# Kernel optimization log

Hardware: AMD Instinct MI355X
Metric: run time of the kernel (lower is better)

## Reference

```python
import jax, jax.numpy as jnp
import numpy as np

N = 200000      # query points
D_IN = 3        # coordinate dims
H = 256         # hidden features
L = 4           # hidden layers (between first and last Perceptron)
S = 8           # n_series == out_features


def setup_inputs() -> dict:
    key = jax.random.key(0)
    ks = jax.random.split(key, 7)
    coords = jax.random.normal(ks[0], (N, D_IN), dtype=jnp.float32)
    # Stacked per-series weights (all series share shapes; original loads the
    # same checkpoint into each, but we use independent random params).
    scale0 = 1.0 / np.sqrt(D_IN)
    scaleh = 1.0 / np.sqrt(H)
    W0 = jax.random.uniform(ks[1], (S, D_IN, H), jnp.float32, -scale0, scale0)
    b0 = jax.random.uniform(ks[2], (S, H), jnp.float32, -scale0, scale0)
    Wh = jax.random.uniform(ks[3], (S, L, H, H), jnp.float32, -scaleh, scaleh)
    bh = jax.random.uniform(ks[4], (S, L, H), jnp.float32, -scaleh, scaleh)
    Wout = jax.random.uniform(ks[5], (S, H, 1), jnp.float32, -scaleh, scaleh)
    bout = jax.random.uniform(ks[6], (S, 1), jnp.float32, -scaleh, scaleh)
    return {"coords": coords, "W0": W0, "b0": b0, "Wh": Wh, "bh": bh,
            "Wout": Wout, "bout": bout}


def reference(coords, W0, b0, Wh, bh, Wout, bout):
    # All S series' MLPs batched into grouped GEMMs (einsum over series axis s).
    # Perceptron = Linear + softplus; last layer is plain Linear.
    h = jax.nn.softplus(jnp.einsum('nd,sdh->snh', coords, W0) + b0[:, None, :])
    for i in range(L):  # small fixed layer count
        h = jax.nn.softplus(
            jnp.einsum('snh,shk->snk', h, Wh[:, i]) + bh[:, i][:, None, :])
    out = jnp.einsum('snh,sho->sno', h, Wout) + bout[:, None, :]  # [S,N,1]
    output = jnp.transpose(out[..., 0], (1, 0))  # concat along dim=1 -> [N,S]
    return (output, coords)
```

## Files before the change

### kernel.cpp

```cpp
#include <hip/hip_runtime.h>
#include <hip/hip_bf16.h>
#include <cstdint>

typedef __attribute__((ext_vector_type(8))) short short8;
typedef __attribute__((ext_vector_type(4))) float float4v;

#define LOG2E 1.44269504088896340736f
#define LN2   0.69314718055994530942f

#if __has_builtin(__builtin_amdgcn_exp2f)
__device__ __forceinline__ float fexp2(float x){ return __builtin_amdgcn_exp2f(x); }
#else
__device__ __forceinline__ float fexp2(float x){ return exp2f(x); }
#endif
#if __has_builtin(__builtin_amdgcn_logf)
__device__ __forceinline__ float flog2(float x){ return __builtin_amdgcn_logf(x); }
#else
__device__ __forceinline__ float flog2(float x){ return log2f(x); }
#endif

__device__ __forceinline__ float softplus_hat(float zh){
  return flog2(1.0f + fexp2(zh));
}

__device__ __forceinline__ unsigned short bf16_trunc(float f){
  return (unsigned short)(__builtin_bit_cast(unsigned int, f) >> 16);
}

#define HSTRIDE 264
#define MISTEP  4288
#define HSIZE   (64 * 264 + 16 * 16)

__global__ void convert_wh(const float* __restrict__ Wh,
                           unsigned short* __restrict__ Wt){
  int e = blockIdx.x * 256 + threadIdx.x;
  int n  = e & 255;
  int k  = (e >> 8) & 255;
  int sl = e >> 16;
  float v = Wh[e];
  __hip_bfloat16 h = __float2bfloat16(v);
  Wt[(sl << 16) + ((k >> 5) << 13) + (n << 5) + (k & 31)] =
      __builtin_bit_cast(unsigned short, h);
}

__device__ __forceinline__ float4v bf16_mfma(short8 a, short8 b, float4v c){
  return __builtin_amdgcn_mfma_f32_16x16x32_bf16(a, b, c, 0, 0, 0);
}

__device__ __forceinline__ void l0_rows(
    unsigned short* __restrict__ ht, const float4v* __restrict__ c4,
    int j, int c, float w0, float w1, float w2, float bb)
{
  float4v x0 = c4[j*3+0], x1 = c4[j*3+1], x2 = c4[j*3+2];
  float z0 = fmaf(x0.z, w2, fmaf(x0.y, w1, fmaf(x0.x, w0, bb)));
  float z1 = fmaf(x1.y, w2, fmaf(x1.x, w1, fmaf(x0.w, w0, bb)));
  float z2 = fmaf(x2.x, w2, fmaf(x1.w, w1, fmaf(x1.z, w0, bb)));
  float z3 = fmaf(x2.w, w2, fmaf(x2.z, w1, fmaf(x2.y, w0, bb)));
  ht[(4*j+0)*HSTRIDE + j*16 + c] = bf16_trunc(softplus_hat(z0));
  ht[(4*j+1)*HSTRIDE + j*16 + c] = bf16_trunc(softplus_hat(z1));
  ht[(4*j+2)*HSTRIDE + j*16 + c] = bf16_trunc(softplus_hat(z2));
  ht[(4*j+3)*HSTRIDE + j*16 + c] = bf16_trunc(softplus_hat(z3));
}

__device__ __forceinline__ void sp2(const float4v (&acc)[4][4],
    unsigned short* __restrict__ cptr, int kb)
{
  #pragma unroll
  for (int t = 0; t < 2; ++t) {
    const int idx = kb * 2 + t, mi = idx >> 2, ni = idx & 3;
    float4v v = acc[mi][ni];
    #pragma unroll
    for (int r = 0; r < 4; ++r)
      cptr[mi * MISTEP + r * HSTRIDE + ni * 16] = bf16_trunc(softplus_hat(v[r]));
  }
}

__device__ __forceinline__ void spdot2(const float4v (&acc)[4][4],
    const float (&wv)[4], float (&p)[16], int kb)
{
  #pragma unroll
  for (int t = 0; t < 2; ++t) {
    const int idx = kb * 2 + t, mi = idx >> 2, ni = idx & 3;
    float4v v = acc[mi][ni];
    #pragma unroll
    for (int r = 0; r < 4; ++r)
      p[mi * 4 + r] = fmaf(softplus_hat(v[r]), wv[ni], p[mi * 4 + r]);
  }
}

template<int PH, bool LOADN, class F>
__device__ __forceinline__ void mfma_phase(
    const unsigned short* __restrict__ bb,
    const unsigned short* __restrict__ bn,
    const unsigned short* __restrict__ aptr,
    short8 (&bq)[3][4], float4v (&acc)[4][4], F&& other)
{
  short8 a0[4], a1[4];
  #pragma unroll
  for (int mi = 0; mi < 4; ++mi)
    a0[mi] = *(const short8*)(aptr + mi * MISTEP);

  #pragma unroll
  for (int kb = 0; kb < 8; ++kb) {
    short8* cur = (kb & 1) ? a1 : a0;
    short8* nxt = (kb & 1) ? a0 : a1;
    if (kb < 7) {
      #pragma unroll
      for (int mi = 0; mi < 4; ++mi)
        nxt[mi] = *(const short8*)(aptr + (kb + 1) * 32 + mi * MISTEP);
    }
    const int slot = (8 * PH + kb) % 3;
    #pragma unroll
    for (int mi = 0; mi < 4; ++mi)
      #pragma unroll
      for (int ni = 0; ni < 4; ++ni)
        acc[mi][ni] = bf16_mfma(cur[mi], bq[slot][ni], acc[mi][ni]);
    if (kb < 5) {
      #pragma unroll
      for (int ni = 0; ni < 4; ++ni)
        bq[slot][ni] = *(const short8*)(bb + (kb + 3) * 8192 + ni * 512);
    } else if (LOADN) {
      #pragma unroll
      for (int ni = 0; ni < 4; ++ni)
        bq[slot][ni] = *(const short8*)(bn + (kb - 5) * 8192 + ni * 512);
    }
    other(kb);
  }
}

__global__ __launch_bounds__(256, 2) void series_mlp(
    const float* __restrict__ coords,
    const float* __restrict__ W0, const float* __restrict__ b0,
    const float* __restrict__ bh,
    const float* __restrict__ Wout, const float* __restrict__ bout,
    const unsigned short* __restrict__ Wt,
    float* __restrict__ out)
{
  __shared__ __align__(16) unsigned short h_lds[2 * HSIZE];
  __shared__ float cbuf[384];

  const int tid  = threadIdx.x;
  const int lane = tid & 63;
  const int wave = tid >> 6;
  const int s    = blockIdx.x & 7;
  const int m0   = (blockIdx.x >> 3) * 128;

  const int q    = lane >> 4;
  const int lr   = lane & 15;
  const int colb = (wave << 6) + lr;

  {
    int i1 = m0 * 3 + tid;
    int i2 = i1 + 256;
    cbuf[tid] = coords[i1 < 599999 ? i1 : 599999];
    if (tid < 128) cbuf[tid + 256] = coords[i2 < 599999 ? i2 : 599999];
  }

  const int c = tid;
  const float w0  = W0[(s * 3 + 0) * 256 + c] * LOG2E;
  const float w1  = W0[(s * 3 + 1) * 256 + c] * LOG2E;
  const float w2  = W0[(s * 3 + 2) * 256 + c] * LOG2E;
  const float bb0 = b0[s * 256 + c] * LOG2E;

  const unsigned short* bbase0 = Wt + ((s << 2) << 16) + (colb << 5) + (q << 3);
  short8 bq[3][4];
  #pragma unroll
  for (int i = 0; i < 3; ++i)
    #pragma unroll
    for (int ni = 0; ni < 4; ++ni)
      bq[i][ni] = *(const short8*)(bbase0 + i * 8192 + ni * 512);

  const unsigned short* aptrA = h_lds + lr * HSTRIDE + (lr >> 2) * 16 + (q << 3);
  const unsigned short* aptrB = aptrA + HSIZE;
  unsigned short* cptrA = h_lds + q * 1072 + colb;
  unsigned short* cptrB = cptrA + HSIZE;

  const float* bh_s = bh + (s << 10);
  const float4v* c4 = (const float4v*)cbuf;

  __syncthreads();
  #pragma unroll
  for (int j = 0; j < 16; ++j)
    l0_rows(h_lds, c4, j, c, w0, w1, w2, bb0);
  __syncthreads();

  float4v accA[4][4], accB[4][4];

#define INIT_ACC(ACC, LIDX)                                                   \
  {                                                                           \
    float bias[4];                                                            \
    _Pragma("unroll")                                                         \
    for (int ni = 0; ni < 4; ++ni)                                            \
      bias[ni] = bh_s[(LIDX) * 256 + colb + ni * 16] * LOG2E;                 \
    _Pragma("unroll")                                                         \
    for (int mi = 0; mi < 4; ++mi)                                            \
      _Pragma("unroll")                                                       \
      for (int ni = 0; ni < 4; ++ni)                                          \
        ACC[mi][ni] = (float4v){bias[ni], bias[ni], bias[ni], bias[ni]};      \
  }

  const unsigned short* B0 = bbase0;
  const unsigned short* B1 = bbase0 + 65536;
  const unsigned short* B2 = bbase0 + 2 * 65536;
  const unsigned short* B3 = bbase0 + 3 * 65536;

  INIT_ACC(accA, 0)
  mfma_phase<0, true>(B0, B0, aptrA, bq, accA, [&](int kb){
    l0_rows(h_lds + HSIZE, c4 + 48, 2 * kb + 0, c, w0, w1, w2, bb0);
    l0_rows(h_lds + HSIZE, c4 + 48, 2 * kb + 1, c, w0, w1, w2, bb0);
  });
  __syncthreads();

  INIT_ACC(accB, 0)
  mfma_phase<1, true>(B0, B1, aptrB, bq, accB,
      [&](int kb){ sp2(accA, cptrA, kb); });
  __syncthreads();

  INIT_ACC(accA, 1)
  mfma_phase<2, true>(B1, B1, aptrA, bq, accA,
      [&](int kb){ sp2(accB, cptrB, kb); });
  __syncthreads();

  INIT_ACC(accB, 1)
  mfma_phase<3, true>(B1, B2, aptrB, bq, accB,
      [&](int kb){ sp2(accA, cptrA, kb); });
  __syncthreads();

  INIT_ACC(accA, 2)
  mfma_phase<4, true>(B2, B2, aptrA, bq, accA,
      [&](int kb){ sp2(accB, cptrB, kb); });
  __syncthreads();

  INIT_ACC(accB, 2)
  mfma_phase<5, true>(B2, B3, aptrB, bq, accB,
      [&](int kb){ sp2(accA, cptrA, kb); });
  __syncthreads();

  INIT_ACC(accA, 3)
  mfma_phase<6, true>(B3, B3, aptrA, bq, accA,
      [&](int kb){ sp2(accB, cptrB, kb); });
  __syncthreads();

  INIT_ACC(accB, 3)
  float wv[4];
  #pragma unroll
  for (int ni = 0; ni < 4; ++ni)
    wv[ni] = Wout[(s << 8) + colb + ni * 16];
  float pA[16], pB[16];
  #pragma unroll
  for (int i = 0; i < 16; ++i) pA[i] = 0.f;
  mfma_phase<7, false>(B3, B3, aptrB, bq, accB,
      [&](int kb){ spdot2(accA, wv, pA, kb); });

  #pragma unroll
  for (int i = 0; i < 16; ++i) pB[i] = 0.f;
  #pragma unroll
  for (int kb = 0; kb < 8; ++kb)
    spdot2(accB, wv, pB, kb);

  __syncthreads();
  float* redA = (float*)h_lds;
  float* redB = redA + 64 * 68;
  #pragma unroll
  for (int mi = 0; mi < 4; ++mi)
    #pragma unroll
    for (int r = 0; r < 4; ++r) {
      int row = mi * 16 + (q << 2) + r;
      redA[row * 68 + (wave << 4) + lr] = pA[mi * 4 + r];
      redB[row * 68 + (wave << 4) + lr] = pB[mi * 4 + r];
    }
  __syncthreads();

  if (tid < 128) {
    const int t = tid & 63;
    const float* red = (tid < 64) ? redA : redB;
    const float4v* rr = (const float4v*)&red[t * 68];
    float4v a = rr[0];
    #pragma unroll
    for (int i = 1; i < 16; ++i) {
      float4v b = rr[i];
      a.x += b.x; a.y += b.y; a.z += b.z; a.w += b.w;
    }
    float tot = (a.x + a.y) + (a.z + a.w);
    int row = m0 + ((tid >> 6) << 6) + t;
    if (row < 200000)
      out[row * 8 + s] = fmaf(LN2, tot, bout[s]);
  }
#undef INIT_ACC
}

__global__ __launch_bounds__(256) void series_mlp_slow(
    const float* __restrict__ coords,
    const float* __restrict__ W0, const float* __restrict__ b0,
    const float* __restrict__ Wh, const float* __restrict__ bh,
    const float* __restrict__ Wout, const float* __restrict__ bout,
    float* __restrict__ out)
{
  __shared__ float hh[64 * 256];
  __shared__ float cbuf[192];
  __shared__ float red[256];
  const int tid = threadIdx.x;
  const int s   = blockIdx.y;
  const int m0  = blockIdx.x * 64;

  if (tid < 192) cbuf[tid] = coords[m0 * 3 + tid];
  __syncthreads();
  {
    const float w0 = W0[(s * 3 + 0) * 256 + tid];
    const float w1 = W0[(s * 3 + 1) * 256 + tid];
    const float w2 = W0[(s * 3 + 2) * 256 + tid];
    const float bb = b0[s * 256 + tid];
    for (int m = 0; m < 64; ++m) {
      float z = fmaf(cbuf[m * 3 + 2], w2,
                fmaf(cbuf[m * 3 + 1], w1,
                fmaf(cbuf[m * 3 + 0], w0, bb)));
      hh[m * 256 + tid] = LN2 * softplus_hat(z * LOG2E);
    }
  }
  __syncthreads();

  for (int l = 0; l < 4; ++l) {
    const float* W = Wh + (((s << 2) + l) << 16);
    const float bb = bh[((s << 2) + l) * 256 + tid];
    float acc[64];
    #pragma unroll
    for (int m = 0; m < 64; ++m) acc[m] = bb;
    for (int kc = 0; kc < 64; ++kc) {
      float w0 = W[(kc * 4 + 0) * 256 + tid];
      float w1 = W[(kc * 4 + 1) * 256 + tid];
      float w2 = W[(kc * 4 + 2) * 256 + tid];
      float w3 = W[(kc * 4 + 3) * 256 + tid];
      #pragma unroll
      for (int m = 0; m < 64; ++m) {
        float4v hv = *(const float4v*)&hh[m * 256 + kc * 4];
        acc[m] = fmaf(hv.w, w3, fmaf(hv.z, w2,
                 fmaf(hv.y, w1, fmaf(hv.x, w0, acc[m]))));
      }
    }
    __syncthreads();
    #pragma unroll
    for (int m = 0; m < 64; ++m)
      hh[m * 256 + tid] = LN2 * softplus_hat(acc[m] * LOG2E);
    __syncthreads();
  }
  {
    const int m = tid >> 2, qq = tid & 3;
    const float* wv = Wout + (s << 8);
    float sum = 0.f;
    for (int i = 0; i < 16; ++i) {
      int kk = (qq << 6) + ((((tid & 15) + i) << 2) & 63);
      float4v hv = *(const float4v*)&hh[m * 256 + kk];
      sum += hv.x * wv[kk] + hv.y * wv[kk + 1] + hv.z * wv[kk + 2] + hv.w * wv[kk + 3];
    }
    red[tid] = sum;
    __syncthreads();
    if (tid < 64)
      out[(m0 + tid) * 8 + s] =
          red[tid * 4] + red[tid * 4 + 1] + red[tid * 4 + 2] + red[tid * 4 + 3] + bout[s];
  }
}

extern "C" void kernel_launch(void* const* d_in, const int* in_sizes, int n_in,
                              void* d_out, int out_size, void* d_ws, size_t ws_size,
                              hipStream_t stream) {
  const float* coords = (const float*)d_in[0];
  const float* W0     = (const float*)d_in[1];
  const float* b0     = (const float*)d_in[2];
  const float* Wh     = (const float*)d_in[3];
  const float* bh     = (const float*)d_in[4];
  const float* Wout   = (const float*)d_in[5];
  const float* bout   = (const float*)d_in[6];
  float* out = (float*)d_out;

  const size_t WT_BYTES = (size_t)8 * 4 * 256 * 256 * 2;
  if (ws_size >= WT_BYTES) {
    unsigned short* Wt = (unsigned short*)d_ws;
    convert_wh<<<8192, 256, 0, stream>>>(Wh, Wt);
    series_mlp<<<dim3(12504), dim3(256), 0, stream>>>(
        coords, W0, b0, bh, Wout, bout, Wt, out);
  } else {
    series_mlp_slow<<<dim3(3125, 8), dim3(256), 0, stream>>>(
        coords, W0, b0, Wh, bh, Wout, bout, out);
  }
  hipMemcpyAsync(out + (size_t)200000 * 8, coords,
                 (size_t)200000 * 3 * sizeof(float),
                 hipMemcpyDeviceToDevice, stream);
}
```

Baseline: 931.8 us.

## Split MFMA and softplus work into producer/consumer wave groups

Blocks grow to 512 threads. Waves 0-3 run only the MFMA GEMMs and write the pre-activation values as fp16 into a double-buffered LDS staging area. Waves 4-7 read those values, apply softplus, and write the bf16 activations for the next layer, so transcendental work overlaps with matrix work across wave groups instead of being interleaved in one wave. The output projection becomes a separate LDS-based dot product at the end. This adds a large amount of LDS (about 70 KB of staging), an extra fp16 rounding of pre-activations, and a block-wide barrier per phase, all of which may lower occupancy.

```diff
diff --git a/kernel.cpp b/kernel.cpp
--- a/kernel.cpp
+++ b/kernel.cpp
@@ -3,6 +3,7 @@
 #include <cstdint>
 
 typedef __attribute__((ext_vector_type(8))) short short8;
+typedef __attribute__((ext_vector_type(4))) short short4v;
 typedef __attribute__((ext_vector_type(4))) float float4v;
 
 #define LOG2E 1.44269504088896340736f
@@ -27,9 +28,21 @@
   return (unsigned short)(__builtin_bit_cast(unsigned int, f) >> 16);
 }
 
+__device__ __forceinline__ unsigned short f16_rne(float f){
+  _Float16 h = (_Float16)f;
+  return __builtin_bit_cast(unsigned short, h);
+}
+__device__ __forceinline__ float f16_to_f32(unsigned short u){
+  _Float16 h = __builtin_bit_cast(_Float16, u);
+  return (float)h;
+}
+
 #define HSTRIDE 264
 #define MISTEP  4288
 #define HSIZE   (64 * 264 + 16 * 16)
+
+#define ZSTRIDE 68
+#define ZSIZE   (256 * ZSTRIDE)
 
 __global__ void convert_wh(const float* __restrict__ Wh,
                            unsigned short* __restrict__ Wt){
@@ -62,38 +75,12 @@
   ht[(4*j+3)*HSTRIDE + j*16 + c] = bf16_trunc(softplus_hat(z3));
 }
 
-__device__ __forceinline__ void sp2(const float4v (&acc)[4][4],
-    unsigned short* __restrict__ cptr, int kb)
-{
-  #pragma unroll
-  for (int t = 0; t < 2; ++t) {
-    const int idx = kb * 2 + t, mi = idx >> 2, ni = idx & 3;
-    float4v v = acc[mi][ni];
-    #pragma unroll
-    for (int r = 0; r < 4; ++r)
-      cptr[mi * MISTEP + r * HSTRIDE + ni * 16] = bf16_trunc(softplus_hat(v[r]));
-  }
-}
-
-__device__ __forceinline__ void spdot2(const float4v (&acc)[4][4],
-    const float (&wv)[4], float (&p)[16], int kb)
-{
-  #pragma unroll
-  for (int t = 0; t < 2; ++t) {
-    const int idx = kb * 2 + t, mi = idx >> 2, ni = idx & 3;
-    float4v v = acc[mi][ni];
-    #pragma unroll
-    for (int r = 0; r < 4; ++r)
-      p[mi * 4 + r] = fmaf(softplus_hat(v[r]), wv[ni], p[mi * 4 + r]);
-  }
-}
-
-template<int PH, bool LOADN, class F>
+template<int PH, bool LOADN>
 __device__ __forceinline__ void mfma_phase(
     const unsigned short* __restrict__ bb,
     const unsigned short* __restrict__ bn,
     const unsigned short* __restrict__ aptr,
-    short8 (&bq)[3][4], float4v (&acc)[4][4], F&& other)
+    short8 (&bq)[3][4], float4v (&acc)[4][4])
 {
   short8 a0[4], a1[4];
   #pragma unroll
@@ -124,11 +111,10 @@
       for (int ni = 0; ni < 4; ++ni)
         bq[slot][ni] = *(const short8*)(bn + (kb - 5) * 8192 + ni * 512);
     }
-    other(kb);
-  }
-}
-
-__global__ __launch_bounds__(256, 2) void series_mlp(
+  }
+}
+
+__global__ __launch_bounds__(512, 2) void series_mlp(
     const float* __restrict__ coords,
     const float* __restrict__ W0, const float* __restrict__ b0,
     const float* __restrict__ bh,
@@ -137,7 +123,9 @@
     float* __restrict__ out)
 {
   __shared__ __align__(16) unsigned short h_lds[2 * HSIZE];
+  __shared__ __align__(16) unsigned short zbuf[2][ZSIZE];
   __shared__ float cbuf[384];
+  __shared__ float wout_s[256];
 
   const int tid  = threadIdx.x;
   const int lane = tid & 63;
@@ -147,46 +135,50 @@
 
   const int q    = lane >> 4;
   const int lr   = lane & 15;
-  const int colb = (wave << 6) + lr;
-
-  {
-    int i1 = m0 * 3 + tid;
-    int i2 = i1 + 256;
-    cbuf[tid] = coords[i1 < 599999 ? i1 : 599999];
-    if (tid < 128) cbuf[tid + 256] = coords[i2 < 599999 ? i2 : 599999];
-  }
-
-  const int c = tid;
-  const float w0  = W0[(s * 3 + 0) * 256 + c] * LOG2E;
-  const float w1  = W0[(s * 3 + 1) * 256 + c] * LOG2E;
-  const float w2  = W0[(s * 3 + 2) * 256 + c] * LOG2E;
-  const float bb0 = b0[s * 256 + c] * LOG2E;
+  const int colb = ((wave & 3) << 6) + lr;
+  const int cc   = tid & 255;
+
+  if (tid < 384) {
+    int idx = m0 * 3 + tid;
+    cbuf[tid] = coords[idx < 599999 ? idx : 599999];
+  }
+  if (tid < 256) wout_s[tid] = Wout[(s << 8) + tid];
 
   const unsigned short* bbase0 = Wt + ((s << 2) << 16) + (colb << 5) + (q << 3);
   short8 bq[3][4];
-  #pragma unroll
-  for (int i = 0; i < 3; ++i)
-    #pragma unroll
-    for (int ni = 0; ni < 4; ++ni)
-      bq[i][ni] = *(const short8*)(bbase0 + i * 8192 + ni * 512);
+  if (wave < 4) {
+    #pragma unroll
+    for (int i = 0; i < 3; ++i)
+      #pragma unroll
+      for (int ni = 0; ni < 4; ++ni)
+        bq[i][ni] = *(const short8*)(bbase0 + i * 8192 + ni * 512);
+  }
 
   const unsigned short* aptrA = h_lds + lr * HSTRIDE + (lr >> 2) * 16 + (q << 3);
   const unsigned short* aptrB = aptrA + HSIZE;
-  unsigned short* cptrA = h_lds + q * 1072 + colb;
-  unsigned short* cptrB = cptrA + HSIZE;
 
   const float* bh_s = bh + (s << 10);
   const float4v* c4 = (const float4v*)cbuf;
 
   __syncthreads();
-  #pragma unroll
-  for (int j = 0; j < 16; ++j)
-    l0_rows(h_lds, c4, j, c, w0, w1, w2, bb0);
-  __syncthreads();
-
-  float4v accA[4][4], accB[4][4];
-
-#define INIT_ACC(ACC, LIDX)                                                   \
+
+  {
+    const int th = tid >> 8;
+    unsigned short* ht = h_lds + th * HSIZE;
+    const float4v* cp = c4 + th * 48;
+    const float w0  = W0[(s * 3 + 0) * 256 + cc] * LOG2E;
+    const float w1  = W0[(s * 3 + 1) * 256 + cc] * LOG2E;
+    const float w2  = W0[(s * 3 + 2) * 256 + cc] * LOG2E;
+    const float bb0 = b0[s * 256 + cc] * LOG2E;
+    #pragma unroll
+    for (int j = 0; j < 16; ++j)
+      l0_rows(ht, cp, j, cc, w0, w1, w2, bb0);
+  }
+  __syncthreads();
+
+  float4v acc[4][4];
+
+#define INIT_ACC(LIDX)                                                        \
   {                                                                           \
     float bias[4];                                                            \
     _Pragma("unroll")                                                         \
@@ -196,7 +188,39 @@
     for (int mi = 0; mi < 4; ++mi)                                            \
       _Pragma("unroll")                                                       \
       for (int ni = 0; ni < 4; ++ni)                                          \
-        ACC[mi][ni] = (float4v){bias[ni], bias[ni], bias[ni], bias[ni]};      \
+        acc[mi][ni] = (float4v){bias[ni], bias[ni], bias[ni], bias[ni]};      \
+  }
+
+#define MFMA_PHASE(PH, BB, BN, LOADN, APTR)                                   \
+  if (wave < 4) {                                                             \
+    INIT_ACC((PH) >> 1)                                                       \
+    mfma_phase<PH, LOADN>(BB, BN, APTR, bq, acc);                             \
+    unsigned short* zp = &zbuf[(PH) & 1][colb * ZSTRIDE + (q << 2)];          \
+    _Pragma("unroll")                                                         \
+    for (int mi = 0; mi < 4; ++mi)                                            \
+      _Pragma("unroll")                                                       \
+      for (int ni = 0; ni < 4; ++ni) {                                        \
+        float4v v = acc[mi][ni];                                              \
+        short4v pk = {(short)f16_rne(v.x), (short)f16_rne(v.y),               \
+                      (short)f16_rne(v.z), (short)f16_rne(v.w)};              \
+        *(short4v*)(zp + ni * (16 * ZSTRIDE) + mi * 16) = pk;                 \
+      }                                                                       \
+  }
+
+#define SP_PHASE(ZI, HT)                                                      \
+  if (wave >= 4) {                                                            \
+    const unsigned short* zp = &zbuf[ZI][cc * ZSTRIDE];                       \
+    unsigned short* ht = (HT);                                                \
+    _Pragma("unroll")                                                         \
+    for (int j = 0; j < 16; ++j) {                                            \
+      short4v zv = *(const short4v*)(zp + j * 4);                             \
+      _Pragma("unroll")                                                       \
+      for (int i = 0; i < 4; ++i) {                                           \
+        const int m = j * 4 + i;                                              \
+        float f = f16_to_f32((unsigned short)zv[i]);                          \
+        ht[m * HSTRIDE + (m >> 2) * 16 + cc] = bf16_trunc(softplus_hat(f));   \
+      }                                                                       \
+    }                                                                         \
   }
 
   const unsigned short* B0 = bbase0;
@@ -204,89 +228,58 @@
   const unsigned short* B2 = bbase0 + 2 * 65536;
   const unsigned short* B3 = bbase0 + 3 * 65536;
 
-  INIT_ACC(accA, 0)
-  mfma_phase<0, true>(B0, B0, aptrA, bq, accA, [&](int kb){
-    l0_rows(h_lds + HSIZE, c4 + 48, 2 * kb + 0, c, w0, w1, w2, bb0);
-    l0_rows(h_lds + HSIZE, c4 + 48, 2 * kb + 1, c, w0, w1, w2, bb0);
-  });
-  __syncthreads();
-
-  INIT_ACC(accB, 0)
-  mfma_phase<1, true>(B0, B1, aptrB, bq, accB,
-      [&](int kb){ sp2(accA, cptrA, kb); });
-  __syncthreads();
-
-  INIT_ACC(accA, 1)
-  mfma_phase<2, true>(B1, B1, aptrA, bq, accA,
-      [&](int kb){ sp2(accB, cptrB, kb); });
-  __syncthreads();
-
-  INIT_ACC(accB, 1)
-  mfma_phase<3, true>(B1, B2, aptrB, bq, accB,
-      [&](int kb){ sp2(accA, cptrA, kb); });
-  __syncthreads();
-
-  INIT_ACC(accA, 2)
-  mfma_phase<4, true>(B2, B2, aptrA, bq, accA,
-      [&](int kb){ sp2(accB, cptrB, kb); });
-  __syncthreads();
-
-  INIT_ACC(accB, 2)
-  mfma_phase<5, true>(B2, B3, aptrB, bq, accB,
-      [&](int kb){ sp2(accA, cptrA, kb); });
-  __syncthreads();
-
-  INIT_ACC(accA, 3)
-  mfma_phase<6, true>(B3, B3, aptrA, bq, accA,
-      [&](int kb){ sp2(accB, cptrB, kb); });
-  __syncthreads();
-
-  INIT_ACC(accB, 3)
-  float wv[4];
-  #pragma unroll
-  for (int ni = 0; ni < 4; ++ni)
-    wv[ni] = Wout[(s << 8) + colb + ni * 16];
-  float pA[16], pB[16];
-  #pragma unroll
-  for (int i = 0; i < 16; ++i) pA[i] = 0.f;
-  mfma_phase<7, false>(B3, B3, aptrB, bq, accB,
-      [&](int kb){ spdot2(accA, wv, pA, kb); });
-
-  #pragma unroll
-  for (int i = 0; i < 16; ++i) pB[i] = 0.f;
-  #pragma unroll
-  for (int kb = 0; kb < 8; ++kb)
-    spdot2(accB, wv, pB, kb);
-
-  __syncthreads();
-  float* redA = (float*)h_lds;
-  float* redB = redA + 64 * 68;
-  #pragma unroll
-  for (int mi = 0; mi < 4; ++mi)
-    #pragma unroll
-    for (int r = 0; r < 4; ++r) {
-      int row = mi * 16 + (q << 2) + r;
-      redA[row * 68 + (wave << 4) + lr] = pA[mi * 4 + r];
-      redB[row * 68 + (wave << 4) + lr] = pB[mi * 4 + r];
-    }
-  __syncthreads();
-
-  if (tid < 128) {
-    const int t = tid & 63;
-    const float* red = (tid < 64) ? redA : redB;
-    const float4v* rr = (const float4v*)&red[t * 68];
-    float4v a = rr[0];
-    #pragma unroll
-    for (int i = 1; i < 16; ++i) {
-      float4v b = rr[i];
-      a.x += b.x; a.y += b.y; a.z += b.z; a.w += b.w;
-    }
-    float tot = (a.x + a.y) + (a.z + a.w);
-    int row = m0 + ((tid >> 6) << 6) + t;
-    if (row < 200000)
-      out[row * 8 + s] = fmaf(LN2, tot, bout[s]);
-  }
+  MFMA_PHASE(0, B0, B0, true,  aptrA)
+  __syncthreads();
+  MFMA_PHASE(1, B0, B1, true,  aptrB)  SP_PHASE(0, h_lds)
+  __syncthreads();
+  MFMA_PHASE(2, B1, B1, true,  aptrA)  SP_PHASE(1, h_lds + HSIZE)
+  __syncthreads();
+  MFMA_PHASE(3, B1, B2, true,  aptrB)  SP_PHASE(0, h_lds)
+  __syncthreads();
+  MFMA_PHASE(4, B2, B2, true,  aptrA)  SP_PHASE(1, h_lds + HSIZE)
+  __syncthreads();
+  MFMA_PHASE(5, B2, B3, true,  aptrB)  SP_PHASE(0, h_lds)
+  __syncthreads();
+  MFMA_PHASE(6, B3, B3, true,  aptrA)  SP_PHASE(1, h_lds + HSIZE)
+  __syncthreads();
+  MFMA_PHASE(7, B3, B3, false, aptrB)  SP_PHASE(0, h_lds)
+  __syncthreads();
+  SP_PHASE(1, h_lds + HSIZE)
+  __syncthreads();
+
+#undef MFMA_PHASE
+#undef SP_PHASE
 #undef INIT_ACC
+
+  {
+    const int rt = tid >> 2;
+    const int qq = tid & 3;
+    const int lm = rt & 63;
+    const unsigned short* hrow = h_lds + (rt >> 6) * HSIZE
+        + lm * HSTRIDE + (lm >> 2) * 16 + qq * 64;
+    float sum = 0.f;
+    #pragma unroll
+    for (int j = 0; j < 8; ++j) {
+      short8 hv = *(const short8*)(hrow + j * 8);
+      #pragma unroll
+      for (int i = 0; i < 8; ++i) {
+        float f = __builtin_bit_cast(float,
+                    (unsigned int)((unsigned short)hv[i]) << 16);
+        sum = fmaf(f, wout_s[qq * 64 + j * 8 + i], sum);
+      }
+    }
+    float* red = (float*)zbuf;
+    red[tid] = sum;
+    __syncthreads();
+    if (tid < 128) {
+      int row = m0 + tid;
+      if (row < 200000) {
+        float4v r4 = ((const float4v*)red)[tid];
+        out[row * 8 + s] =
+            fmaf(LN2, (r4.x + r4.y) + (r4.z + r4.w), bout[s]);
+      }
+    }
+  }
 }
 
 __global__ __launch_bounds__(256) void series_mlp_slow(
@@ -376,7 +369,7 @@
   if (ws_size >= WT_BYTES) {
     unsigned short* Wt = (unsigned short*)d_ws;
     convert_wh<<<8192, 256, 0, stream>>>(Wh, Wt);
-    series_mlp<<<dim3(12504), dim3(256), 0, stream>>>(
+    series_mlp<<<dim3(12504), dim3(512), 0, stream>>>(
         coords, W0, b0, bh, Wout, bout, Wt, out);
   } else {
     series_mlp_slow<<<dim3(3125, 8), dim3(256), 0, stream>>>(
```

Measured after the change: 1.389 ms. 49.0% more time.

## Switch hidden-layer GEMMs to 32x32x16 bf16 MFMA with re-laid-out fragments

Applied to the files above, without the earlier changes.

Replaces the 16x16x32 bf16 MFMA tiling (4x4 accumulators per wave) with 32x32x16 MFMA (2x2 accumulators of 16 floats). It remaps the A/B fragment loads, the softplus writeback layout and the final Wout reduction to match the new register layout. Per-layer biases and Wout are hoisted into registers, and sched_barriers fence the interleaved epilogue work. The larger instruction halves the number of operand loads per FLOP, at the cost of a different LDS access pattern and possible bank conflicts or register pressure.

```diff
diff --git a/kernel.cpp b/kernel.cpp
--- a/kernel.cpp
+++ b/kernel.cpp
@@ -4,6 +4,7 @@
 
 typedef __attribute__((ext_vector_type(8))) short short8;
 typedef __attribute__((ext_vector_type(4))) float float4v;
+typedef __attribute__((ext_vector_type(16))) float f32x16;
 
 #define LOG2E 1.44269504088896340736f
 #define LN2   0.69314718055994530942f
@@ -28,7 +29,7 @@
 }
 
 #define HSTRIDE 264
-#define MISTEP  4288
+#define MISTEP32 8576
 #define HSIZE   (64 * 264 + 16 * 16)
 
 __global__ void convert_wh(const float* __restrict__ Wh,
@@ -43,8 +44,8 @@
       __builtin_bit_cast(unsigned short, h);
 }
 
-__device__ __forceinline__ float4v bf16_mfma(short8 a, short8 b, float4v c){
-  return __builtin_amdgcn_mfma_f32_16x16x32_bf16(a, b, c, 0, 0, 0);
+__device__ __forceinline__ f32x16 bf16_mfma32(short8 a, short8 b, f32x16 c){
+  return __builtin_amdgcn_mfma_f32_32x32x16_bf16(a, b, c, 0, 0, 0);
 }
 
 __device__ __forceinline__ void l0_rows(
@@ -62,30 +63,26 @@
   ht[(4*j+3)*HSTRIDE + j*16 + c] = bf16_trunc(softplus_hat(z3));
 }
 
-__device__ __forceinline__ void sp2(const float4v (&acc)[4][4],
-    unsigned short* __restrict__ cptr, int kb)
-{
-  #pragma unroll
-  for (int t = 0; t < 2; ++t) {
-    const int idx = kb * 2 + t, mi = idx >> 2, ni = idx & 3;
-    float4v v = acc[mi][ni];
-    #pragma unroll
-    for (int r = 0; r < 4; ++r)
-      cptr[mi * MISTEP + r * HSTRIDE + ni * 16] = bf16_trunc(softplus_hat(v[r]));
-  }
-}
-
-__device__ __forceinline__ void spdot2(const float4v (&acc)[4][4],
-    const float (&wv)[4], float (&p)[16], int kb)
-{
-  #pragma unroll
-  for (int t = 0; t < 2; ++t) {
-    const int idx = kb * 2 + t, mi = idx >> 2, ni = idx & 3;
-    float4v v = acc[mi][ni];
-    #pragma unroll
-    for (int r = 0; r < 4; ++r)
-      p[mi * 4 + r] = fmaf(softplus_hat(v[r]), wv[ni], p[mi * 4 + r]);
-  }
+__device__ __forceinline__ void sp32(const f32x16 (&acc)[2][2],
+    unsigned short* __restrict__ cptr, int st)
+{
+  const int mi = st >> 3, ni = (st >> 2) & 1, q4 = st & 3;
+  f32x16 v = acc[mi][ni];
+  #pragma unroll
+  for (int r = 0; r < 4; ++r)
+    cptr[ni*32 + q4*2144 + r*264 + mi*MISTEP32] =
+        bf16_trunc(softplus_hat(v[q4*4 + r]));
+}
+
+__device__ __forceinline__ void spdot32(const f32x16 (&acc)[2][2],
+    const float (&wv)[2], float (&p)[32], int st)
+{
+  const int mi = st >> 3, ni = (st >> 2) & 1, q4 = st & 3;
+  f32x16 v = acc[mi][ni];
+  #pragma unroll
+  for (int r = 0; r < 4; ++r)
+    p[mi*16 + q4*4 + r] = fmaf(softplus_hat(v[q4*4 + r]), wv[ni],
+                               p[mi*16 + q4*4 + r]);
 }
 
 template<int PH, bool LOADN, class F>
@@ -93,38 +90,41 @@
     const unsigned short* __restrict__ bb,
     const unsigned short* __restrict__ bn,
     const unsigned short* __restrict__ aptr,
-    short8 (&bq)[3][4], float4v (&acc)[4][4], F&& other)
-{
-  short8 a0[4], a1[4];
-  #pragma unroll
-  for (int mi = 0; mi < 4; ++mi)
-    a0[mi] = *(const short8*)(aptr + mi * MISTEP);
-
-  #pragma unroll
-  for (int kb = 0; kb < 8; ++kb) {
-    short8* cur = (kb & 1) ? a1 : a0;
-    short8* nxt = (kb & 1) ? a0 : a1;
-    if (kb < 7) {
+    short8 (&bq)[3][2], f32x16 (&acc)[2][2], F&& other)
+{
+  short8 a0[2], a1[2];
+  #pragma unroll
+  for (int mi = 0; mi < 2; ++mi)
+    a0[mi] = *(const short8*)(aptr + mi * MISTEP32);
+
+  #pragma unroll
+  for (int st = 0; st < 16; ++st) {
+    short8* cur = (st & 1) ? a1 : a0;
+    short8* nxt = (st & 1) ? a0 : a1;
+    const int slot = (16 * PH + st) % 3;
+    acc[0][0] = bf16_mfma32(cur[0], bq[slot][0], acc[0][0]);
+    acc[0][1] = bf16_mfma32(cur[0], bq[slot][1], acc[0][1]);
+    acc[1][0] = bf16_mfma32(cur[1], bq[slot][0], acc[1][0]);
+    acc[1][1] = bf16_mfma32(cur[1], bq[slot][1], acc[1][1]);
+    if (st < 15) {
       #pragma unroll
-      for (int mi = 0; mi < 4; ++mi)
-        nxt[mi] = *(const short8*)(aptr + (kb + 1) * 32 + mi * MISTEP);
-    }
-    const int slot = (8 * PH + kb) % 3;
-    #pragma unroll
-    for (int mi = 0; mi < 4; ++mi)
+      for (int mi = 0; mi < 2; ++mi)
+        nxt[mi] = *(const short8*)(aptr + (st + 1) * 16 + mi * MISTEP32);
+    }
+    if (st < 13) {
       #pragma unroll
-      for (int ni = 0; ni < 4; ++ni)
-        acc[mi][ni] = bf16_mfma(cur[mi], bq[slot][ni], acc[mi][ni]);
-    if (kb < 5) {
-      #pragma unroll
-      for (int ni = 0; ni < 4; ++ni)
-        bq[slot][ni] = *(const short8*)(bb + (kb + 3) * 8192 + ni * 512);
+      for (int ni = 0; ni < 2; ++ni)
+        bq[slot][ni] = *(const short8*)(bb + ((st + 3) >> 1) * 8192 +
+                                        ni * 1024 + ((st + 3) & 1) * 16);
     } else if (LOADN) {
       #pragma unroll
-      for (int ni = 0; ni < 4; ++ni)
-        bq[slot][ni] = *(const short8*)(bn + (kb - 5) * 8192 + ni * 512);
-    }
-    other(kb);
+      for (int ni = 0; ni < 2; ++ni)
+        bq[slot][ni] = *(const short8*)(bn + ((st - 13) >> 1) * 8192 +
+                                        ni * 1024 + ((st - 13) & 1) * 16);
+    }
+    __builtin_amdgcn_sched_barrier(0);
+    other(st);
+    __builtin_amdgcn_sched_barrier(0);
   }
 }
 
@@ -145,9 +145,8 @@
   const int s    = blockIdx.x & 7;
   const int m0   = (blockIdx.x >> 3) * 128;
 
-  const int q    = lane >> 4;
-  const int lr   = lane & 15;
-  const int colb = (wave << 6) + lr;
+  const int l31  = lane & 31;
+  const int lh   = lane >> 5;
 
   {
     int i1 = m0 * 3 + tid;
@@ -162,20 +161,34 @@
   const float w2  = W0[(s * 3 + 2) * 256 + c] * LOG2E;
   const float bb0 = b0[s * 256 + c] * LOG2E;
 
-  const unsigned short* bbase0 = Wt + ((s << 2) << 16) + (colb << 5) + (q << 3);
-  short8 bq[3][4];
+  const unsigned short* bbase0 =
+      Wt + ((s << 2) << 16) + ((wave << 6) + l31) * 32 + (lh << 3);
+  short8 bq[3][2];
   #pragma unroll
   for (int i = 0; i < 3; ++i)
     #pragma unroll
-    for (int ni = 0; ni < 4; ++ni)
-      bq[i][ni] = *(const short8*)(bbase0 + i * 8192 + ni * 512);
-
-  const unsigned short* aptrA = h_lds + lr * HSTRIDE + (lr >> 2) * 16 + (q << 3);
+    for (int ni = 0; ni < 2; ++ni)
+      bq[i][ni] = *(const short8*)(bbase0 + (i >> 1) * 8192 + ni * 1024 +
+                                   (i & 1) * 16);
+
+  const float* bh_s = bh + (s << 10);
+  float bias_r[4][2];
+  #pragma unroll
+  for (int l = 0; l < 4; ++l)
+    #pragma unroll
+    for (int ni = 0; ni < 2; ++ni)
+      bias_r[l][ni] = bh_s[l * 256 + (wave << 6) + ni * 32 + l31] * LOG2E;
+  float wv[2];
+  #pragma unroll
+  for (int ni = 0; ni < 2; ++ni)
+    wv[ni] = Wout[(s << 8) + (wave << 6) + ni * 32 + l31];
+
+  const unsigned short* aptrA =
+      h_lds + l31 * HSTRIDE + (l31 >> 2) * 16 + (lh << 3);
   const unsigned short* aptrB = aptrA + HSIZE;
-  unsigned short* cptrA = h_lds + q * 1072 + colb;
+  unsigned short* cptrA = h_lds + (wave << 6) + l31 + lh * 1072;
   unsigned short* cptrB = cptrA + HSIZE;
 
-  const float* bh_s = bh + (s << 10);
   const float4v* c4 = (const float4v*)cbuf;
 
   __syncthreads();
@@ -184,19 +197,18 @@
     l0_rows(h_lds, c4, j, c, w0, w1, w2, bb0);
   __syncthreads();
 
-  float4v accA[4][4], accB[4][4];
+  f32x16 accA[2][2], accB[2][2];
 
 #define INIT_ACC(ACC, LIDX)                                                   \
   {                                                                           \
-    float bias[4];                                                            \
     _Pragma("unroll")                                                         \
-    for (int ni = 0; ni < 4; ++ni)                                            \
-      bias[ni] = bh_s[(LIDX) * 256 + colb + ni * 16] * LOG2E;                 \
-    _Pragma("unroll")                                                         \
-    for (int mi = 0; mi < 4; ++mi)                                            \
+    for (int mi = 0; mi < 2; ++mi)                                            \
       _Pragma("unroll")                                                       \
-      for (int ni = 0; ni < 4; ++ni)                                          \
-        ACC[mi][ni] = (float4v){bias[ni], bias[ni], bias[ni], bias[ni]};      \
+      for (int ni = 0; ni < 2; ++ni) {                                        \
+        float bv = bias_r[LIDX][ni];                                          \
+        _Pragma("unroll")                                                     \
+        for (int r = 0; r < 16; ++r) ACC[mi][ni][r] = bv;                     \
+      }                                                                       \
   }
 
   const unsigned short* B0 = bbase0;
@@ -205,86 +217,88 @@
   const unsigned short* B3 = bbase0 + 3 * 65536;
 
   INIT_ACC(accA, 0)
-  mfma_phase<0, true>(B0, B0, aptrA, bq, accA, [&](int kb){
-    l0_rows(h_lds + HSIZE, c4 + 48, 2 * kb + 0, c, w0, w1, w2, bb0);
-    l0_rows(h_lds + HSIZE, c4 + 48, 2 * kb + 1, c, w0, w1, w2, bb0);
+  mfma_phase<0, true>(B0, B0, aptrA, bq, accA, [&](int st){
+    l0_rows(h_lds + HSIZE, c4 + 48, st, c, w0, w1, w2, bb0);
   });
   __syncthreads();
 
   INIT_ACC(accB, 0)
   mfma_phase<1, true>(B0, B1, aptrB, bq, accB,
-      [&](int kb){ sp2(accA, cptrA, kb); });
+      [&](int st){ sp32(accA, cptrA, st); });
   __syncthreads();
 
   INIT_ACC(accA, 1)
   mfma_phase<2, true>(B1, B1, aptrA, bq, accA,
-      [&](int kb){ sp2(accB, cptrB, kb); });
+      [&](int st){ sp32(accB, cptrB, st); });
   __syncthreads();
 
   INIT_ACC(accB, 1)
   mfma_phase<3, true>(B1, B2, aptrB, bq, accB,
-      [&](int kb){ sp2(accA, cptrA, kb); });
+      [&](int st){ sp32(accA, cptrA, st); });
   __syncthreads();
 
   INIT_ACC(accA, 2)
   mfma_phase<4, true>(B2, B2, aptrA, bq, accA,
-      [&](int kb){ sp2(accB, cptrB, kb); });
+      [&](int st){ sp32(accB, cptrB, st); });
   __syncthreads();
 
   INIT_ACC(accB, 2)
   mfma_phase<5, true>(B2, B3, aptrB, bq, accB,
-      [&](int kb){ sp2(accA, cptrA, kb); });
+      [&](int st){ sp32(accA, cptrA, st); });
   __syncthreads();
 
   INIT_ACC(accA, 3)
   mfma_phase<6, true>(B3, B3, aptrA, bq, accA,
-      [&](int kb){ sp2(accB, cptrB, kb); });
+      [&](int st){ sp32(accB, cptrB, st); });
   __syncthreads();
 
   INIT_ACC(accB, 3)
-  float wv[4];
-  #pragma unroll
-  for (int ni = 0; ni < 4; ++ni)
-    wv[ni] = Wout[(s << 8) + colb + ni * 16];
-  float pA[16], pB[16];
-  #pragma unroll
-  for (int i = 0; i < 16; ++i) pA[i] = 0.f;
+  float pA[32], pB[32];
+  #pragma unroll
+  for (int i = 0; i < 32; ++i) pA[i] = 0.f;
   mfma_phase<7, false>(B3, B3, aptrB, bq, accB,
-      [&](int kb){ spdot2(accA, wv, pA, kb); });
-
-  #pragma unroll
-  for (int i = 0; i < 16; ++i) pB[i] = 0.f;
-  #pragma unroll
-  for (int kb = 0; kb < 8; ++kb)
-    spdot2(accB, wv, pB, kb);
+      [&](int st){ spdot32(accA, wv, pA, st); });
+
+  #pragma unroll
+  for (int i = 0; i < 32; ++i) pB[i] = 0.f;
+  #pragma unroll
+  for (int st = 0; st < 16; ++st)
+    spdot32(accB, wv, pB, st);
 
   __syncthreads();
   float* redA = (float*)h_lds;
-  float* redB = redA + 64 * 68;
-  #pragma unroll
-  for (int mi = 0; mi < 4; ++mi)
-    #pragma unroll
-    for (int r = 0; r < 4; ++r) {
-      int row = mi * 16 + (q << 2) + r;
-      redA[row * 68 + (wave << 4) + lr] = pA[mi * 4 + r];
-      redB[row * 68 + (wave << 4) + lr] = pB[mi * 4 + r];
-    }
-  __syncthreads();
-
-  if (tid < 128) {
-    const int t = tid & 63;
-    const float* red = (tid < 64) ? redA : redB;
-    const float4v* rr = (const float4v*)&red[t * 68];
+  float* redB = (float*)(h_lds + HSIZE);
+  const int rbase = lh * 528 + (wave << 5) + l31;
+  #pragma unroll
+  for (int mi = 0; mi < 2; ++mi)
+    #pragma unroll
+    for (int q4 = 0; q4 < 4; ++q4)
+      #pragma unroll
+      for (int r = 0; r < 4; ++r) {
+        const int sl = mi * 16 + q4 * 4 + r;
+        const int mb = mi * 32 + q4 * 8 + r;
+        redA[mb * 132 + rbase] = pA[sl];
+        redB[mb * 132 + rbase] = pB[sl];
+      }
+  __syncthreads();
+
+  {
+    const int rowg = tid >> 1, half = tid & 1;
+    const float* red = (rowg < 64) ? redA : redB;
+    const float4v* rr = (const float4v*)&red[(rowg & 63) * 132 + half * 64];
     float4v a = rr[0];
     #pragma unroll
     for (int i = 1; i < 16; ++i) {
       float4v b = rr[i];
       a.x += b.x; a.y += b.y; a.z += b.z; a.w += b.w;
     }
-    float tot = (a.x + a.y) + (a.z + a.w);
-    int row = m0 + ((tid >> 6) << 6) + t;
-    if (row < 200000)
-      out[row * 8 + s] = fmaf(LN2, tot, bout[s]);
+    float hsum = (a.x + a.y) + (a.z + a.w);
+    float tot = hsum + __shfl_xor(hsum, 1);
+    if (half == 0) {
+      int row = m0 + rowg;
+      if (row < 200000)
+        out[row * 8 + s] = fmaf(LN2, tot, bout[s]);
+    }
   }
 #undef INIT_ACC
 }
```

New measurement: 1.040 ms. +11.6%, slower.
